# Optimization experiments

Measured on AMD Instinct MI355X. Metric: run time of the kernel, lower is better.

Reference implementation:

```python
import jax, jax.numpy as jnp
import numpy as np


def setup_inputs() -> dict:
    key = jax.random.key(0)
    k1, k2 = jax.random.split(key)
    B, N, D = 4, 4096, 128
    E = jax.random.normal(k1, (B, N, D), dtype=jnp.float32)
    W = jax.random.normal(k2, (1, 2 * D), dtype=jnp.float32) * (1.0 / np.sqrt(2 * D))
    return {"E": E, "W": W}


def reference(E, W):
    # Original: pairs[b,i,j] = concat(E[b,i], E[b,j]); score = pairs @ W.T
    # Equivalent: score[b,i,j] = E[b,i] . W[:, :D] + E[b,j] . W[:, D:]
    D = E.shape[-1]
    w_i = W[0, :D]   # (D,)
    w_j = W[0, D:]   # (D,)
    a = jnp.einsum("bnd,d->bn", E, w_i)  # per-node row scalar
    b = jnp.einsum("bnd,d->bn", E, w_j)  # per-node col scalar
    return a[:, :, None] + b[:, None, :]  # (B, N, N)
```

## Files before the change

### kernel.cpp

```cpp
#include <hip/hip_runtime.h>

constexpr int BATCH = 4;
constexpr int N = 4096;
constexpr int D = 128;

typedef float vfloat4 __attribute__((ext_vector_type(4)));

__global__ void dots_kernel(const float* __restrict__ E,
                            const float* __restrict__ W,
                            float* __restrict__ A,
                            float* __restrict__ Bv) {
    const int gtid = blockIdx.x * blockDim.x + threadIdx.x;
    const int wave = gtid >> 6;
    const int lane = threadIdx.x & 63;
    if (wave >= BATCH * N) return;

    const float* row = E + (size_t)wave * D;
    const float2 e  = *reinterpret_cast<const float2*>(row + lane * 2);
    const float2 wi = *reinterpret_cast<const float2*>(W + lane * 2);
    const float2 wj = *reinterpret_cast<const float2*>(W + D + lane * 2);

    float pa = e.x * wi.x + e.y * wi.y;
    float pb = e.x * wj.x + e.y * wj.y;

    #pragma unroll
    for (int off = 32; off >= 1; off >>= 1) {
        pa += __shfl_xor(pa, off);
        pb += __shfl_xor(pb, off);
    }
    if (lane == 0) {
        A[wave]  = pa;
        Bv[wave] = pb;
    }
}

__global__ void outer_kernel(const float* __restrict__ A,
                             const float* __restrict__ Bv,
                             vfloat4* __restrict__ out) {
    constexpr int J4 = N / 4;
    const size_t total4 = (size_t)BATCH * N * J4;
    const size_t stride = (size_t)gridDim.x * blockDim.x;

    for (size_t idx = (size_t)blockIdx.x * blockDim.x + threadIdx.x;
         idx < total4; idx += stride) {
        const int j4    = (int)(idx & (J4 - 1));
        const int i     = (int)((idx >> 10) & (N - 1));
        const int batch = (int)(idx >> 22);

        const float a = A[batch * N + i];
        const vfloat4 b4 = reinterpret_cast<const vfloat4*>(Bv)[batch * J4 + j4];

        vfloat4 v;
        v.x = a + b4.x;
        v.y = a + b4.y;
        v.z = a + b4.z;
        v.w = a + b4.w;
        __builtin_nontemporal_store(v, &out[idx]);
    }
}

extern "C" void kernel_launch(void* const* d_in, const int* in_sizes, int n_in,
                              void* d_out, int out_size, void* d_ws, size_t ws_size,
                              hipStream_t stream) {
    const float* E = (const float*)d_in[0];
    const float* W = (const float*)d_in[1];

    float* A  = (float*)d_ws;
    float* Bv = A + (size_t)BATCH * N;

    {
        const int threads = 256;
        const int rows = BATCH * N;
        const int blocks = rows / (threads / 64);
        dots_kernel<<<blocks, threads, 0, stream>>>(E, W, A, Bv);
    }

    {
        const int threads = 256;
        const int blocks = 4096;
        outer_kernel<<<blocks, threads, 0, stream>>>(A, Bv, (vfloat4*)d_out);
    }
}
```

Before: 60.79 us.

## Fuse dot products and outer sum into one tiled kernel

Replaces the two-kernel pipeline (per-row dot products to workspace, then broadcast add) with a single kernel. Each block handles a 512x512 output tile, computes the needed row and column dot products into LDS, then writes the tile. This removes a kernel launch and the workspace round trip. In exchange, each row's dot product is recomputed once per tile (8 times), with one thread serially reading a full 128-float row using strided, poorly coalesced loads. The nontemporal stores are also replaced by plain stores.

```diff
diff --git a/kernel.cpp b/kernel.cpp
--- a/kernel.cpp
+++ b/kernel.cpp
@@ -3,59 +3,63 @@
 constexpr int BATCH = 4;
 constexpr int N = 4096;
 constexpr int D = 128;
+constexpr int TILE = 512;
+constexpr int NT = N / TILE;
 
 typedef float vfloat4 __attribute__((ext_vector_type(4)));
 
-__global__ void dots_kernel(const float* __restrict__ E,
-                            const float* __restrict__ W,
-                            float* __restrict__ A,
-                            float* __restrict__ Bv) {
-    const int gtid = blockIdx.x * blockDim.x + threadIdx.x;
-    const int wave = gtid >> 6;
-    const int lane = threadIdx.x & 63;
-    if (wave >= BATCH * N) return;
-
-    const float* row = E + (size_t)wave * D;
-    const float2 e  = *reinterpret_cast<const float2*>(row + lane * 2);
-    const float2 wi = *reinterpret_cast<const float2*>(W + lane * 2);
-    const float2 wj = *reinterpret_cast<const float2*>(W + D + lane * 2);
-
-    float pa = e.x * wi.x + e.y * wi.y;
-    float pb = e.x * wj.x + e.y * wj.y;
-
+__device__ __forceinline__ float dot_row(const float* __restrict__ row,
+                                         const float* __restrict__ w) {
+    float acc = 0.f;
     #pragma unroll
-    for (int off = 32; off >= 1; off >>= 1) {
-        pa += __shfl_xor(pa, off);
-        pb += __shfl_xor(pb, off);
+    for (int c = 0; c < D / 4; ++c) {
+        const vfloat4 e  = reinterpret_cast<const vfloat4*>(row)[c];
+        const vfloat4 wv = reinterpret_cast<const vfloat4*>(w)[c];
+        acc += e.x * wv.x + e.y * wv.y + e.z * wv.z + e.w * wv.w;
     }
-    if (lane == 0) {
-        A[wave]  = pa;
-        Bv[wave] = pb;
-    }
+    return acc;
 }
 
-__global__ void outer_kernel(const float* __restrict__ A,
-                             const float* __restrict__ Bv,
-                             vfloat4* __restrict__ out) {
-    constexpr int J4 = N / 4;
-    const size_t total4 = (size_t)BATCH * N * J4;
-    const size_t stride = (size_t)gridDim.x * blockDim.x;
+__global__ __launch_bounds__(256)
+void fused_kernel(const float* __restrict__ E,
+                  const float* __restrict__ W,
+                  vfloat4* __restrict__ out) {
+    __shared__ float a_lds[TILE];
+    __shared__ float b_lds[TILE];
 
-    for (size_t idx = (size_t)blockIdx.x * blockDim.x + threadIdx.x;
-         idx < total4; idx += stride) {
-        const int j4    = (int)(idx & (J4 - 1));
-        const int i     = (int)((idx >> 10) & (N - 1));
-        const int batch = (int)(idx >> 22);
+    const int bx    = blockIdx.x;
+    const int batch = bx >> 6;
+    const int ti    = (bx >> 3) & (NT - 1);
+    const int tj    = bx & (NT - 1);
+    const int t     = threadIdx.x;
 
-        const float a = A[batch * N + i];
-        const vfloat4 b4 = reinterpret_cast<const vfloat4*>(Bv)[batch * J4 + j4];
+    const float* Eb = E + (size_t)batch * N * D;
+    const float* Wa = W;
+    const float* Wb = W + D;
 
-        vfloat4 v;
-        v.x = a + b4.x;
-        v.y = a + b4.y;
-        v.z = a + b4.z;
-        v.w = a + b4.w;
-        __builtin_nontemporal_store(v, &out[idx]);
+    const int i0 = ti * TILE;
+    const int j0 = tj * TILE;
+
+    a_lds[t]       = dot_row(Eb + (size_t)(i0 + t) * D,       Wa);
+    a_lds[t + 256] = dot_row(Eb + (size_t)(i0 + t + 256) * D, Wa);
+    b_lds[t]       = dot_row(Eb + (size_t)(j0 + t) * D,       Wb);
+    b_lds[t + 256] = dot_row(Eb + (size_t)(j0 + t + 256) * D, Wb);
+    __syncthreads();
+
+    const int j4 = t & 63;
+    const int r0 = t >> 6;
+    const vfloat4 b4_0 = reinterpret_cast<const vfloat4*>(b_lds)[j4];
+    const vfloat4 b4_1 = reinterpret_cast<const vfloat4*>(b_lds)[j4 + 64];
+
+    vfloat4* outb = out + ((size_t)batch * N + i0) * (N / 4) + (size_t)tj * (TILE / 4);
+
+    #pragma unroll 4
+    for (int k = 0; k < TILE / 4; ++k) {
+        const int row = r0 + k * 4;
+        const float a = a_lds[row];
+        vfloat4* orow = outb + (size_t)row * (N / 4);
+        orow[j4]      = b4_0 + a;
+        orow[j4 + 64] = b4_1 + a;
     }
 }
 
@@ -65,19 +69,5 @@
     const float* E = (const float*)d_in[0];
     const float* W = (const float*)d_in[1];
 
-    float* A  = (float*)d_ws;
-    float* Bv = A + (size_t)BATCH * N;
-
-    {
-        const int threads = 256;
-        const int rows = BATCH * N;
-        const int blocks = rows / (threads / 64);
-        dots_kernel<<<blocks, threads, 0, stream>>>(E, W, A, Bv);
-    }
-
-    {
-        const int threads = 256;
-        const int blocks = 4096;
-        outer_kernel<<<blocks, threads, 0, stream>>>(A, Bv, (vfloat4*)d_out);
-    }
+    fused_kernel<<<BATCH * NT * NT, 256, 0, stream>>>(E, W, (vfloat4*)d_out);
 }
```

Measured after the change: 71.79 us. 18.1% more time.
